# Kernel optimization log

Hardware: AMD Instinct MI355X
Metric: run time of the kernel (lower is better)

The kernel has to match this reference:

```python
import jax, jax.numpy as jnp
import numpy as np
from jax import lax

WINDOW_RADIUS = 8  # model_config['window_radius']


def _layernorm(x, g, b, eps=1e-5):
    mu = jnp.mean(x, axis=-1, keepdims=True)
    var = jnp.var(x, axis=-1, keepdims=True)
    return (x - mu) * lax.rsqrt(var + eps) * g + b


def setup_inputs() -> dict:
    key = jax.random.key(0)
    ks = jax.random.split(key, 8)
    B, T, D = 4, 2048, 1024
    d_b, d_k, KV = 256, 128, 48
    d_in = D + d_b + d_k  # 1408
    s = 1.0 / np.sqrt(D)
    return {
        "h": jax.random.normal(ks[0], (B, T, D), jnp.float32),
        "bound_w": jax.random.normal(ks[1], (D,), jnp.float32) * s,
        "bound_b": jnp.zeros((1,), jnp.float32),
        "conv_w": jax.random.normal(ks[2], (9,), jnp.float32) * (1.0 / 3.0),
        "conv_b": jnp.zeros((1,), jnp.float32),
        "e0": jnp.zeros((d_b,), jnp.float32),
        "e1": jax.random.normal(ks[3], (d_b,), jnp.float32) * 0.02,
        "key_emb": jax.random.normal(ks[4], (KV, d_k), jnp.float32),
        "key_w": jax.random.normal(ks[5], (D, KV), jnp.float32) * s,
        "key_b": jnp.zeros((KV,), jnp.float32),
        "ln_in_g": jnp.ones((d_in,), jnp.float32),
        "ln_in_b": jnp.zeros((d_in,), jnp.float32),
        "film_w": jax.random.normal(ks[6], (d_in, 2 * D), jnp.float32) * (1.0 / np.sqrt(d_in)),
        "film_b": jnp.zeros((2 * D,), jnp.float32),
        "ln_h_g": jnp.ones((D,), jnp.float32),
        "ln_h_b": jnp.zeros((D,), jnp.float32),
    }


def reference(h, bound_w, bound_b, conv_w, conv_b, e0, e1, key_emb, key_w, key_b,
              ln_in_g, ln_in_b, film_w, film_b, ln_h_g, ln_h_b):
    B, T, D = h.shape
    R = WINDOW_RADIUS
    # boundary head + Conv1d(1,1,k,padding=k//2) smoother + sigmoid
    boundary_logits = jnp.einsum('btd,d->bt', h, bound_w) + bound_b[0]  # [B,T]
    kb = conv_w.shape[0]
    sm = lax.conv_general_dilated(boundary_logits[:, None, :], conv_w[None, None, :],
                                  window_strides=(1,), padding=[(kb // 2, kb // 2)])
    b_soft = jax.nn.sigmoid(sm[:, 0, :] + conv_b[0])  # [B,T]
    # key conditioning: softmax over key logits, soft-mix of key embedding table
    key_soft = jax.nn.softmax(jnp.einsum('btd,dk->btk', h, key_w) + key_b, axis=-1)
    ek = jnp.einsum('btk,ke->bte', key_soft, key_emb)  # [B,T,d_k]
    # boundary embedding interpolation
    eb = b_soft[..., None] * e1 + (1.0 - b_soft[..., None]) * e0  # [B,T,d_b]
    # FiLM: concat + LN + Linear -> gamma/beta, modulate LN(h)
    film_in = _layernorm(jnp.concatenate([h, eb, ek], axis=-1), ln_in_g, ln_in_b)
    gb = jnp.einsum('bti,io->bto', film_in, film_w) + film_b  # [B,T,2D]
    gamma, beta = gb[..., :D], gb[..., D:]
    z = _layernorm(h, ln_h_g, ln_h_b) * (1.0 + gamma) + beta  # [B,T,D]
    # local windows: replicate-pad along T, im2col-style gather of width 2R+1
    padded = jnp.pad(h, ((0, 0), (R, R), (0, 0)), mode='edge')  # [B,T+2R,D]
    idx = jnp.arange(T)[:, None] + jnp.arange(2 * R + 1)[None, :]  # [T,W]
    win = padded[:, idx, :]  # [B,T,W,D]
    C = jnp.concatenate([z[:, :, None, :], win], axis=2)  # [B,T,W+1,D]
    return C
```

## Files before the change

### kernel.cpp

```cpp
#include <hip/hip_runtime.h>
#include <math.h>

#define B_    4
#define T_    2048
#define D_    1024
#define DB_   256
#define DKk_  128
#define KV_   48
#define DIN_  1408
#define NT_   (B_ * T_)
#define RAD_  8

#define OFS_BOUND  0
#define OFS_BSOFT  8192
#define OFS_KEY    16384
#define OFS_EK     409600
#define OFS_HSTAT  1458176
#define OFS_BF16   1474560
#define UOFS_AHI   0u
#define UOFS_ALO   11534336u
#define UOFS_BHI   23068672u
#define UOFS_BLO   25952256u

typedef __attribute__((ext_vector_type(8))) short s16x8;
typedef __attribute__((ext_vector_type(4))) float f32x4;

__device__ __forceinline__ unsigned short f2bf(float f) {
    unsigned u; __builtin_memcpy(&u, &f, 4);
    u += 0x7fffu + ((u >> 16) & 1u);
    return (unsigned short)(u >> 16);
}
__device__ __forceinline__ unsigned short f2bf_hi(float f, float* back) {
    unsigned u; __builtin_memcpy(&u, &f, 4);
    u += 0x7fffu + ((u >> 16) & 1u);
    unsigned short h = (unsigned short)(u >> 16);
    unsigned hb = (unsigned)h << 16;
    __builtin_memcpy(back, &hb, 4);
    return h;
}
__device__ __forceinline__ void gload_lds16(const void* g, void* s) {
    __builtin_amdgcn_global_load_lds(
        (const __attribute__((address_space(1))) unsigned int*)g,
        (__attribute__((address_space(3))) unsigned int*)s,
        16, 0, 0);
}

__global__ __launch_bounds__(256) void k_prepw(
    const float* __restrict__ film_w, unsigned short* __restrict__ Bhi,
    unsigned short* __restrict__ Blo)
{
    __shared__ float tile[32][33];
    const int n0 = blockIdx.x * 32;
    const int k0 = blockIdx.y * 32;
    const int tid = threadIdx.x;
    const int c = tid & 31, r0 = tid >> 5;
    #pragma unroll
    for (int i = 0; i < 4; ++i) {
        int r = r0 + i * 8;
        tile[r][c] = film_w[(size_t)(k0 + r) * 2048 + n0 + c];
    }
    __syncthreads();
    #pragma unroll
    for (int i = 0; i < 4; ++i) {
        int rn = r0 + i * 8;
        float f = tile[c][rn];
        float fh;
        unsigned short hs = f2bf_hi(f, &fh);
        unsigned short ls = f2bf(f - fh);
        Bhi[(size_t)(n0 + rn) * 1408 + k0 + c] = hs;
        Blo[(size_t)(n0 + rn) * 1408 + k0 + c] = ls;
    }
}

__global__ __launch_bounds__(256) void k_logits(
    const float* __restrict__ h, const float* __restrict__ bound_w,
    const float* __restrict__ bound_b, const float* __restrict__ key_w,
    const float* __restrict__ key_b, float* __restrict__ ws)
{
    __shared__ __align__(16) float As[32][68];
    __shared__ float Ws[64][64];
    const int tid  = threadIdx.x;
    const int tok0 = blockIdx.x * 32;
    const int c  = tid & 63;
    const int rg = tid >> 6;
    const int arow = tid >> 3;
    const int akb  = (tid & 7) * 8;
    float acc[8] = {0,0,0,0,0,0,0,0};

    for (int kc = 0; kc < 1024; kc += 64) {
        {
            const float* src = &h[(size_t)(tok0 + arow) * 1024 + kc + akb];
            float4 a0 = *(const float4*)(src);
            float4 a1 = *(const float4*)(src + 4);
            *(float4*)&As[arow][akb]     = a0;
            *(float4*)&As[arow][akb + 4] = a1;
        }
        #pragma unroll
        for (int i = 0; i < 12; ++i) {
            int l = tid + 256 * i;
            int r = l / 48, cc = l - r * 48;
            Ws[r][cc] = key_w[(size_t)(kc + r) * 48 + cc];
        }
        if (tid < 64) Ws[tid][48] = bound_w[kc + tid];
        __syncthreads();
        #pragma unroll
        for (int kk4 = 0; kk4 < 16; ++kk4) {
            float w0 = Ws[kk4 * 4 + 0][c];
            float w1 = Ws[kk4 * 4 + 1][c];
            float w2 = Ws[kk4 * 4 + 2][c];
            float w3 = Ws[kk4 * 4 + 3][c];
            #pragma unroll
            for (int i = 0; i < 8; ++i) {
                float4 a = *(const float4*)&As[rg * 8 + i][kk4 * 4];
                acc[i] += a.x * w0 + a.y * w1 + a.z * w2 + a.w * w3;
            }
        }
        __syncthreads();
    }

    if (c < 48) {
        float kb = key_b[c];
        #pragma unroll
        for (int i = 0; i < 8; ++i)
            ws[OFS_KEY + (size_t)(tok0 + rg * 8 + i) * 48 + c] = acc[i] + kb;
    } else if (c == 48) {
        float bb = bound_b[0];
        #pragma unroll
        for (int i = 0; i < 8; ++i)
            ws[OFS_BOUND + tok0 + rg * 8 + i] = acc[i] + bb;
    }
}

__global__ __launch_bounds__(256) void k_conv(
    const float* __restrict__ conv_w, const float* __restrict__ conv_b,
    float* __restrict__ ws)
{
    int id = blockIdx.x * 256 + threadIdx.x;
    if (id >= NT_) return;
    int b = id >> 11, t = id & 2047;
    float s = conv_b[0];
    #pragma unroll
    for (int i = 0; i < 9; ++i) {
        int tt = t + i - 4;
        if (tt >= 0 && tt < T_) s += ws[OFS_BOUND + b * T_ + tt] * conv_w[i];
    }
    ws[OFS_BSOFT + id] = 1.0f / (1.0f + expf(-s));
}

__global__ __launch_bounds__(128) void k_softek(
    const float* __restrict__ key_emb, float* __restrict__ ws)
{
    __shared__ float p[48];
    const int tok = blockIdx.x;
    const int tid = threadIdx.x;
    if (tid < 64) {
        float v = (tid < 48) ? ws[OFS_KEY + (size_t)tok * 48 + tid] : -1e30f;
        float m = v;
        #pragma unroll
        for (int off = 32; off; off >>= 1) m = fmaxf(m, __shfl_xor(m, off, 64));
        float e = (tid < 48) ? expf(v - m) : 0.0f;
        float s = e;
        #pragma unroll
        for (int off = 32; off; off >>= 1) s += __shfl_xor(s, off, 64);
        if (tid < 48) p[tid] = e / s;
    }
    __syncthreads();
    float acc = 0.0f;
    #pragma unroll 8
    for (int k = 0; k < 48; ++k) acc += p[k] * key_emb[k * 128 + tid];
    ws[OFS_EK + (size_t)tok * 128 + tid] = acc;
}

__global__ __launch_bounds__(256) void k_filmin(
    const float* __restrict__ h, const float* __restrict__ e0,
    const float* __restrict__ e1, const float* __restrict__ ln_in_g,
    const float* __restrict__ ln_in_b, float* __restrict__ ws,
    unsigned short* __restrict__ Ahi, unsigned short* __restrict__ Alo)
{
    const int tok = blockIdx.x;
    const int tid = threadIdx.x;
    const float bs = ws[OFS_BSOFT + tok];
    float val[6];
    float s_all = 0.f, ss_all = 0.f, s_h = 0.f, ss_h = 0.f;
    int n = 0;
    for (int j = tid; j < DIN_; j += 256, ++n) {
        float v;
        if (j < 1024)       v = h[(size_t)tok * 1024 + j];
        else if (j < 1280)  { int i = j - 1024; v = bs * e1[i] + (1.0f - bs) * e0[i]; }
        else                v = ws[OFS_EK + (size_t)tok * 128 + (j - 1280)];
        val[n] = v;
        s_all += v; ss_all += v * v;
        if (j < 1024) { s_h += v; ss_h += v * v; }
    }
    #pragma unroll
    for (int off = 32; off; off >>= 1) {
        s_all  += __shfl_down(s_all, off);
        ss_all += __shfl_down(ss_all, off);
        s_h    += __shfl_down(s_h, off);
        ss_h   += __shfl_down(ss_h, off);
    }
    __shared__ float red[4][4];
    const int wid = tid >> 6;
    if ((tid & 63) == 0) {
        red[wid][0] = s_all; red[wid][1] = ss_all;
        red[wid][2] = s_h;   red[wid][3] = ss_h;
    }
    __syncthreads();
    float S   = red[0][0] + red[1][0] + red[2][0] + red[3][0];
    float SS  = red[0][1] + red[1][1] + red[2][1] + red[3][1];
    float Sh  = red[0][2] + red[1][2] + red[2][2] + red[3][2];
    float SSh = red[0][3] + red[1][3] + red[2][3] + red[3][3];
    float mean  = S * (1.0f / 1408.0f);
    float var   = SS * (1.0f / 1408.0f) - mean * mean;
    float rstd  = rsqrtf(var + 1e-5f);
    float mean_h = Sh * (1.0f / 1024.0f);
    float var_h  = SSh * (1.0f / 1024.0f) - mean_h * mean_h;
    float rstd_h = rsqrtf(var_h + 1e-5f);
    if (tid == 0) {
        ws[OFS_HSTAT + tok * 2]     = mean_h;
        ws[OFS_HSTAT + tok * 2 + 1] = rstd_h;
    }
    n = 0;
    for (int j = tid; j < DIN_; j += 256, ++n) {
        float f = (val[n] - mean) * rstd * ln_in_g[j] + ln_in_b[j];
        float fh;
        unsigned short hs = f2bf_hi(f, &fh);
        Ahi[(size_t)tok * 1408 + j] = hs;
        Alo[(size_t)tok * 1408 + j] = f2bf(f - fh);
    }
}

__global__ __launch_bounds__(256) void k_gemm_mfma(
    const unsigned short* __restrict__ Ahi, const unsigned short* __restrict__ Alo,
    const unsigned short* __restrict__ Bhi, const unsigned short* __restrict__ Blo,
    const float* __restrict__ film_b, const float* __restrict__ h,
    const float* __restrict__ hstat, const float* __restrict__ ln_h_g,
    const float* __restrict__ ln_h_b, float* __restrict__ out)
{
    __shared__ __align__(16) char lds[65536];
    const int tid  = threadIdx.x;
    const int wg   = blockIdx.x;
    const int swz  = (wg & 7) * 128 + (wg >> 3);
    const int m0   = (swz & 63) * 128;
    const int n0   = (swz >> 6) * 64;
    const int lane = tid & 63;
    const int wid  = tid >> 6;
    const int wm   = wid >> 1, wn = wid & 1;
    const int lr   = lane & 15;
    const int hi16 = ((lane >> 4) & 3) * 16;
    const int sa   = (lr & 7) << 4;
    const int srow = tid >> 3;
    const int sswz = ((((tid & 7) * 16) ^ ((srow & 7) << 4)) >> 1);
    const int sdst = tid * 16;

    f32x4 accg[4][2] = {};
    f32x4 accb[4][2] = {};

    auto stage = [&](int cc, int bufi) {
        const unsigned short* Ap = (cc < 22) ? Ahi : (cc < 44 ? Alo : Ahi);
        const unsigned short* Bp = (cc < 44) ? Bhi : Blo;
        const int kc = (cc >= 44 ? cc - 44 : (cc >= 22 ? cc - 22 : cc)) * 64;
        char* base = lds + bufi * 32768;
        #pragma unroll
        for (int c = 0; c < 4; ++c) {
            gload_lds16(Ap + (size_t)(m0 + srow + c * 32) * 1408 + kc + sswz,
                        base + c * 4096 + sdst);
            int r = srow + c * 32;
            int col = n0 + r + ((r >> 6) * 960);
            gload_lds16(Bp + (size_t)col * 1408 + kc + sswz,
                        base + 16384 + c * 4096 + sdst);
        }
    };

    stage(0, 0);
    __syncthreads();

    for (int cc = 0; cc < 66; ++cc) {
        const int cur = cc & 1;
        if (cc + 1 < 66) stage(cc + 1, cur ^ 1);
        const char* base = lds + cur * 32768;
        #pragma unroll
        for (int ks = 0; ks < 2; ++ks) {
            s16x8 af[4], bg[2], bb[2];
            const int koff = (ks * 64 + hi16) ^ sa;
            #pragma unroll
            for (int mt = 0; mt < 4; ++mt) {
                int row = wm * 64 + mt * 16 + lr;
                af[mt] = *(const s16x8*)(base + row * 128 + koff);
            }
            #pragma unroll
            for (int nt = 0; nt < 2; ++nt) {
                int rg = wn * 32 + nt * 16 + lr;
                bg[nt] = *(const s16x8*)(base + 16384 + rg * 128 + koff);
                bb[nt] = *(const s16x8*)(base + 16384 + (rg + 64) * 128 + koff);
            }
            #pragma unroll
            for (int mt = 0; mt < 4; ++mt)
                #pragma unroll
                for (int nt = 0; nt < 2; ++nt) {
                    accg[mt][nt] = __builtin_amdgcn_mfma_f32_16x16x32_bf16(
                        af[mt], bg[nt], accg[mt][nt], 0, 0, 0);
                    accb[mt][nt] = __builtin_amdgcn_mfma_f32_16x16x32_bf16(
                        af[mt], bb[nt], accb[mt][nt], 0, 0, 0);
                }
        }
        __syncthreads();
    }

    #pragma unroll
    for (int mt = 0; mt < 4; ++mt) {
        #pragma unroll
        for (int r = 0; r < 4; ++r) {
            const int tok = m0 + wm * 64 + mt * 16 + ((lane >> 4) & 3) * 4 + r;
            const float mh = hstat[tok * 2], rh = hstat[tok * 2 + 1];
            #pragma unroll
            for (int nt = 0; nt < 2; ++nt) {
                const int nc = n0 + wn * 32 + nt * 16 + lr;
                float g  = accg[mt][nt][r] + film_b[nc];
                float bt = accb[mt][nt][r] + film_b[1024 + nc];
                float hv = h[(size_t)tok * 1024 + nc];
                float lnh = (hv - mh) * rh * ln_h_g[nc] + ln_h_b[nc];
                out[(size_t)tok * (18 * 1024) + nc] = lnh * (1.0f + g) + bt;
            }
        }
    }
}

__global__ __launch_bounds__(256) void k_window(
    const float* __restrict__ h, float* __restrict__ out)
{
    const int tokg = blockIdx.x;
    const int t = tokg & 2047, b = tokg >> 11;
    float4* dst = (float4*)&out[(size_t)tokg * 18 * 1024];
    #pragma unroll 4
    for (int slot = 0; slot < 17; ++slot) {
        int st = t + slot - RAD_;
        st = st < 0 ? 0 : (st > T_ - 1 ? T_ - 1 : st);
        const float4* src = (const float4*)&h[(size_t)(b * T_ + st) * 1024];
        dst[(1 + slot) * 256 + threadIdx.x] = src[threadIdx.x];
    }
}

extern "C" void kernel_launch(void* const* d_in, const int* in_sizes, int n_in,
                              void* d_out, int out_size, void* d_ws, size_t ws_size,
                              hipStream_t stream)
{
    const float* h       = (const float*)d_in[0];
    const float* bound_w = (const float*)d_in[1];
    const float* bound_b = (const float*)d_in[2];
    const float* conv_w  = (const float*)d_in[3];
    const float* conv_b  = (const float*)d_in[4];
    const float* e0      = (const float*)d_in[5];
    const float* e1      = (const float*)d_in[6];
    const float* key_emb = (const float*)d_in[7];
    const float* key_w   = (const float*)d_in[8];
    const float* key_b   = (const float*)d_in[9];
    const float* ln_in_g = (const float*)d_in[10];
    const float* ln_in_b = (const float*)d_in[11];
    const float* film_w  = (const float*)d_in[12];
    const float* film_b  = (const float*)d_in[13];
    const float* ln_h_g  = (const float*)d_in[14];
    const float* ln_h_b  = (const float*)d_in[15];
    float* ws  = (float*)d_ws;
    float* out = (float*)d_out;
    unsigned short* ub  = (unsigned short*)(ws + OFS_BF16);
    unsigned short* Ahi = ub + UOFS_AHI;
    unsigned short* Alo = ub + UOFS_ALO;
    unsigned short* Bhi = ub + UOFS_BHI;
    unsigned short* Blo = ub + UOFS_BLO;

    hipLaunchKernelGGL(k_prepw, dim3(64, 44), dim3(256), 0, stream,
                       film_w, Bhi, Blo);
    hipLaunchKernelGGL(k_logits, dim3(NT_ / 32), dim3(256), 0, stream,
                       h, bound_w, bound_b, key_w, key_b, ws);
    hipLaunchKernelGGL(k_conv, dim3(NT_ / 256), dim3(256), 0, stream,
                       conv_w, conv_b, ws);
    hipLaunchKernelGGL(k_softek, dim3(NT_), dim3(128), 0, stream, key_emb, ws);
    hipLaunchKernelGGL(k_filmin, dim3(NT_), dim3(256), 0, stream,
                       h, e0, e1, ln_in_g, ln_in_b, ws, Ahi, Alo);
    hipLaunchKernelGGL(k_gemm_mfma, dim3(1024), dim3(256), 0, stream,
                       Ahi, Alo, Bhi, Blo, film_b, h, ws + OFS_HSTAT,
                       ln_h_g, ln_h_b, out);
    hipLaunchKernelGGL(k_window, dim3(NT_), dim3(256), 0, stream, h, out);
}
```

Before: 961.1 us.

## Restructure split-bf16 GEMM to stage hi/lo together with fragment-ordered LDS layout

```diff
diff --git a/kernel.cpp b/kernel.cpp
--- a/kernel.cpp
+++ b/kernel.cpp
@@ -239,72 +239,84 @@
 {
     __shared__ __align__(16) char lds[65536];
     const int tid  = threadIdx.x;
-    const int wg   = blockIdx.x;
-    const int swz  = (wg & 7) * 128 + (wg >> 3);
-    const int m0   = (swz & 63) * 128;
-    const int n0   = (swz >> 6) * 64;
+    const int m0   = blockIdx.x * 128;
+    const int n0   = blockIdx.y * 64;
     const int lane = tid & 63;
     const int wid  = tid >> 6;
     const int wm   = wid >> 1, wn = wid & 1;
     const int lr   = lane & 15;
-    const int hi16 = ((lane >> 4) & 3) * 16;
-    const int sa   = (lr & 7) << 4;
-    const int srow = tid >> 3;
-    const int sswz = ((((tid & 7) * 16) ^ ((srow & 7) << 4)) >> 1);
-    const int sdst = tid * 16;
 
     f32x4 accg[4][2] = {};
     f32x4 accb[4][2] = {};
 
-    auto stage = [&](int cc, int bufi) {
-        const unsigned short* Ap = (cc < 22) ? Ahi : (cc < 44 ? Alo : Ahi);
-        const unsigned short* Bp = (cc < 44) ? Bhi : Blo;
-        const int kc = (cc >= 44 ? cc - 44 : (cc >= 22 ? cc - 22 : cc)) * 64;
-        char* base = lds + bufi * 32768;
-        #pragma unroll
-        for (int c = 0; c < 4; ++c) {
-            gload_lds16(Ap + (size_t)(m0 + srow + c * 32) * 1408 + kc + sswz,
-                        base + c * 4096 + sdst);
-            int r = srow + c * 32;
-            int col = n0 + r + ((r >> 6) * 960);
-            gload_lds16(Bp + (size_t)col * 1408 + kc + sswz,
-                        base + 16384 + c * 4096 + sdst);
+    auto stage = [&](int s, int bufi) {
+        char* base = lds + (bufi << 15);
+        const int k0 = s * 32;
+        #pragma unroll
+        for (int i = 0; i < 2; ++i) {
+            int f    = tid + (i << 8);
+            int row  = ((f >> 6) << 4) + (f & 15);
+            int koff = k0 + (((f >> 4) & 3) << 3);
+            gload_lds16(Ahi + (size_t)(m0 + row) * 1408 + koff, base + f * 16);
+            gload_lds16(Alo + (size_t)(m0 + row) * 1408 + koff, base + 8192 + f * 16);
+        }
+        {
+            int f    = tid;
+            int rowB = (((f >> 6) & 3) << 4) + (f & 15);
+            int koff = k0 + (((f >> 4) & 3) << 3);
+            gload_lds16(Bhi + (size_t)(n0 + rowB) * 1408 + koff,        base + 16384 + f * 16);
+            gload_lds16(Bhi + (size_t)(1024 + n0 + rowB) * 1408 + koff, base + 20480 + f * 16);
+            gload_lds16(Blo + (size_t)(n0 + rowB) * 1408 + koff,        base + 24576 + f * 16);
+            gload_lds16(Blo + (size_t)(1024 + n0 + rowB) * 1408 + koff, base + 28672 + f * 16);
         }
     };
 
     stage(0, 0);
-    __syncthreads();
-
-    for (int cc = 0; cc < 66; ++cc) {
-        const int cur = cc & 1;
-        if (cc + 1 < 66) stage(cc + 1, cur ^ 1);
-        const char* base = lds + cur * 32768;
-        #pragma unroll
-        for (int ks = 0; ks < 2; ++ks) {
-            s16x8 af[4], bg[2], bb[2];
-            const int koff = (ks * 64 + hi16) ^ sa;
-            #pragma unroll
-            for (int mt = 0; mt < 4; ++mt) {
-                int row = wm * 64 + mt * 16 + lr;
-                af[mt] = *(const s16x8*)(base + row * 128 + koff);
-            }
+
+    for (int s = 0; s < 44; ++s) {
+        if (s + 1 < 44) {
+            stage(s + 1, (s + 1) & 1);
+            asm volatile("s_waitcnt vmcnt(8)" ::: "memory");
+        } else {
+            asm volatile("s_waitcnt vmcnt(0)" ::: "memory");
+        }
+        asm volatile("s_barrier" ::: "memory");
+
+        const char* base = lds + ((s & 1) << 15);
+        s16x8 ah[4], al[4], bgh[2], bbh[2], bgl[2], bbl[2];
+        #pragma unroll
+        for (int mt = 0; mt < 4; ++mt) {
+            int o = ((wm * 4 + mt) << 10) + lane * 16;
+            ah[mt] = *(const s16x8*)(base + o);
+            al[mt] = *(const s16x8*)(base + 8192 + o);
+        }
+        #pragma unroll
+        for (int nt = 0; nt < 2; ++nt) {
+            int o = ((wn * 2 + nt) << 10) + lane * 16;
+            bgh[nt] = *(const s16x8*)(base + 16384 + o);
+            bbh[nt] = *(const s16x8*)(base + 20480 + o);
+            bgl[nt] = *(const s16x8*)(base + 24576 + o);
+            bbl[nt] = *(const s16x8*)(base + 28672 + o);
+        }
+        #pragma unroll
+        for (int mt = 0; mt < 4; ++mt)
             #pragma unroll
             for (int nt = 0; nt < 2; ++nt) {
-                int rg = wn * 32 + nt * 16 + lr;
-                bg[nt] = *(const s16x8*)(base + 16384 + rg * 128 + koff);
-                bb[nt] = *(const s16x8*)(base + 16384 + (rg + 64) * 128 + koff);
+                accg[mt][nt] = __builtin_amdgcn_mfma_f32_16x16x32_bf16(
+                    ah[mt], bgh[nt], accg[mt][nt], 0, 0, 0);
+                accg[mt][nt] = __builtin_amdgcn_mfma_f32_16x16x32_bf16(
+                    al[mt], bgh[nt], accg[mt][nt], 0, 0, 0);
+                accg[mt][nt] = __builtin_amdgcn_mfma_f32_16x16x32_bf16(
+                    ah[mt], bgl[nt], accg[mt][nt], 0, 0, 0);
+                accb[mt][nt] = __builtin_amdgcn_mfma_f32_16x16x32_bf16(
+                    ah[mt], bbh[nt], accb[mt][nt], 0, 0, 0);
+                accb[mt][nt] = __builtin_amdgcn_mfma_f32_16x16x32_bf16(
+                    al[mt], bbh[nt], accb[mt][nt], 0, 0, 0);
+                accb[mt][nt] = __builtin_amdgcn_mfma_f32_16x16x32_bf16(
+                    ah[mt], bbl[nt], accb[mt][nt], 0, 0, 0);
             }
-            #pragma unroll
-            for (int mt = 0; mt < 4; ++mt)
-                #pragma unroll
-                for (int nt = 0; nt < 2; ++nt) {
-                    accg[mt][nt] = __builtin_amdgcn_mfma_f32_16x16x32_bf16(
-                        af[mt], bg[nt], accg[mt][nt], 0, 0, 0);
-                    accb[mt][nt] = __builtin_amdgcn_mfma_f32_16x16x32_bf16(
-                        af[mt], bb[nt], accb[mt][nt], 0, 0, 0);
-                }
-        }
-        __syncthreads();
+
+        asm volatile("s_barrier" ::: "memory");
     }
 
     #pragma unroll
@@ -378,7 +390,7 @@
     hipLaunchKernelGGL(k_softek, dim3(NT_), dim3(128), 0, stream, key_emb, ws);
     hipLaunchKernelGGL(k_filmin, dim3(NT_), dim3(256), 0, stream,
                        h, e0, e1, ln_in_g, ln_in_b, ws, Ahi, Alo);
-    hipLaunchKernelGGL(k_gemm_mfma, dim3(1024), dim3(256), 0, stream,
+    hipLaunchKernelGGL(k_gemm_mfma, dim3(64, 16), dim3(256), 0, stream,
                        Ahi, Alo, Bhi, Blo, film_b, h, ws + OFS_HSTAT,
                        ln_h_g, ln_h_b, out);
     hipLaunchKernelGGL(k_window, dim3(NT_), dim3(256), 0, stream, h, out);
```

New measurement: 971.4 us. About the same (+1.1%).
